# Optimization experiments

Measured on AMD Instinct MI355X. Metric: run time of the kernel, lower is better.

The kernel has to match this reference:

```python
import jax, jax.numpy as jnp
import numpy as np

B, C_IN, N = 32, 64, 128
OUT_FEATS = (64, 64, 128)
ATT_DIM = 64
EPS = 1e-5  # torch BatchNorm default


def _bn(x, g, b, m, v):
    # eval-mode BatchNorm over channel axis 1 (running stats m, v)
    shape = (1, -1) + (1,) * (x.ndim - 2)
    inv = g / jnp.sqrt(v + EPS)
    return (x - m.reshape(shape)) * inv.reshape(shape) + b.reshape(shape)


def setup_inputs() -> dict:
    key = jax.random.key(0)
    ks = iter(jax.random.split(key, 48))

    def w(shape, scale=0.05):
        return jax.random.normal(next(ks), shape, jnp.float32) * scale

    inp = {"features": jax.random.normal(next(ks), (B, C_IN, N), jnp.float32)}
    in_dims = (2 * C_IN, OUT_FEATS[0], OUT_FEATS[1])
    for li in range(3):
        o, ci = OUT_FEATS[li], in_dims[li]
        inp[f"w{li}"] = w((o, ci))                  # Conv2d 1x1, no bias (BN)
        inp[f"g{li}"] = 1.0 + w((o,))               # BN gamma
        inp[f"b{li}"] = w((o,))                     # BN beta
        inp[f"m{li}"] = w((o,))                     # BN running mean
        inp[f"v{li}"] = 1.0 + 0.1 * jax.random.uniform(next(ks), (o,), jnp.float32)
    inp["wa0"] = w((ATT_DIM, OUT_FEATS[-1]))        # attention conv (no bias)
    inp["ga"] = 1.0 + w((ATT_DIM,))
    inp["ba"] = w((ATT_DIM,))
    inp["ma"] = w((ATT_DIM,))
    inp["va"] = 1.0 + 0.1 * jax.random.uniform(next(ks), (ATT_DIM,), jnp.float32)
    inp["wa1"] = w((1, ATT_DIM))                    # final attention conv (bias)
    inp["ba1"] = w((1,))
    inp["wsc"] = w((OUT_FEATS[-1], C_IN))           # shortcut Conv1d (no bias)
    inp["gsc"] = 1.0 + w((OUT_FEATS[-1],))
    inp["bsc"] = w((OUT_FEATS[-1],))
    inp["msc"] = w((OUT_FEATS[-1],))
    inp["vsc"] = 1.0 + 0.1 * jax.random.uniform(next(ks), (OUT_FEATS[-1],), jnp.float32)
    return inp


def reference(features, w0, g0, b0, m0, v0, w1, g1, b1, m1, v1,
              w2, g2, b2, m2, v2, wa0, ga, ba, ma, va, wa1, ba1,
              wsc, gsc, bsc, msc, vsc):
    n = features.shape[-1]
    # neighbor index table: row i lists all j != i, shape (N, N-1)
    base = jnp.broadcast_to(jnp.arange(n)[None, :], (n, n))
    idx = jnp.where(base >= jnp.arange(n)[:, None], base + 1, base)[:, :-1]
    x_i = features[:, :, :, None]                   # (B,C,N,1)
    x_j = features[:, :, idx]                       # (B,C,N,N-1) gather
    x = jnp.concatenate([jnp.broadcast_to(x_i, x_j.shape), x_j - x_i], axis=1)  # (B,2C,N,N-1)
    for w_, g_, b_, m_, v_ in ((w0, g0, b0, m0, v0), (w1, g1, b1, m1, v1), (w2, g2, b2, m2, v2)):
        x = jnp.einsum('oc,bcnk->bonk', w_, x)      # 1x1 conv
        x = jax.nn.relu(_bn(x, g_, b_, m_, v_))
    # attention pooling over neighbor axis k
    a = jax.nn.relu(_bn(jnp.einsum('oc,bcnk->bonk', wa0, x), ga, ba, ma, va))
    logits = jnp.einsum('oc,bcnk->bonk', wa1, a) + ba1.reshape(1, 1, 1, 1)
    attw = jax.nn.softmax(logits[:, 0], axis=-1)    # (B,N,N-1)
    fts = jnp.einsum('bcnk,bnk->bcn', x, attw)      # (B,C_out,N)
    # shortcut branch (in_feat != out_feats[-1])
    sc = _bn(jnp.einsum('oc,bcn->bon', wsc, features), gsc, bsc, msc, vsc)
    return jax.nn.relu(sc + fts)
```

## Files before the change

### kernel.cpp

```cpp
#include <hip/hip_runtime.h>

typedef unsigned short u16;
typedef short short8 __attribute__((ext_vector_type(8)));
typedef float floatx4 __attribute__((ext_vector_type(4)));
typedef __bf16 bf16x2 __attribute__((ext_vector_type(2)));

#define MFMA16(a, b, c) __builtin_amdgcn_mfma_f32_16x16x32_bf16((a), (b), (c), 0, 0, 0)

#define W1F_OFF   0u
#define B1F_OFF   8192u
#define W2F_OFF   8448u
#define B2F_OFF   24832u
#define WA0F_OFF  25344u
#define BAF_OFF   41728u
#define WA1F_OFF  41984u
#define BA1F_OFF  42240u
#define P_OFF     42496u
#define Q_OFF     1091072u
#define SC_OFF    2139648u
#define WS_TOTAL  4236800u

__device__ __align__(256) char g_ws[WS_TOTAL];

#define LD0 72
#define LD2 136

__device__ __forceinline__ float bits2f(unsigned u) {
  union { unsigned i; float f; } v; v.i = u; return v.f;
}
__device__ __forceinline__ unsigned f2bits(float f) {
  union { float f; unsigned i; } v; v.f = f; return v.i;
}
__device__ __forceinline__ u16 f2bf(float f) {
  return (u16)((f2bits(f) + 0x8000u) >> 16);
}
__device__ __forceinline__ unsigned pack2relu(float a, float b) {
#if __has_builtin(__builtin_amdgcn_cvt_pk_bf16_f32)
  union { bf16x2 h; unsigned u; } cv;
  cv.h = __builtin_amdgcn_cvt_pk_bf16_f32(fmaxf(a, 0.f), fmaxf(b, 0.f));
  return cv.u;
#else
  unsigned lo = (f2bits(fmaxf(a, 0.f)) + 0x8000u) >> 16;
  unsigned hi = (f2bits(fmaxf(b, 0.f)) + 0x8000u) & 0xffff0000u;
  return lo | hi;
#endif
}

__global__ __launch_bounds__(256) void k_pre(
    const float* __restrict__ feat, const float* __restrict__ w0,
    const float* __restrict__ g0, const float* __restrict__ b0, const float* __restrict__ m0, const float* __restrict__ v0,
    const float* __restrict__ w1, const float* __restrict__ g1, const float* __restrict__ b1, const float* __restrict__ m1, const float* __restrict__ v1,
    const float* __restrict__ w2, const float* __restrict__ g2, const float* __restrict__ b2, const float* __restrict__ m2, const float* __restrict__ v2,
    const float* __restrict__ wa0, const float* __restrict__ ga, const float* __restrict__ ba, const float* __restrict__ ma, const float* __restrict__ va,
    const float* __restrict__ wa1, const float* __restrict__ ba1,
    const float* __restrict__ wsc, const float* __restrict__ gsc, const float* __restrict__ bsc, const float* __restrict__ msc, const float* __restrict__ vsc)
{
  __shared__ float smem[9600];
  const int t = threadIdx.x;
  char* ws = g_ws;
  const int blk = blockIdx.x;

  if (blk == 512) {
    float* fs1 = smem; float* fs2 = smem + 64; float* fsa = smem + 192;
    if (t < 64) {
      float s;
      s = g1[t] * rsqrtf(v1[t] + 1e-5f); fs1[t] = s; ((float*)(ws + B1F_OFF))[t] = b1[t] - m1[t] * s;
      s = ga[t] * rsqrtf(va[t] + 1e-5f); fsa[t] = s; ((float*)(ws + BAF_OFF))[t] = ba[t] - ma[t] * s;
      ((float*)(ws + WA1F_OFF))[t] = wa1[t];
    }
    if (t < 128) { float s = g2[t] * rsqrtf(v2[t] + 1e-5f); fs2[t] = s; ((float*)(ws + B2F_OFF))[t] = b2[t] - m2[t] * s; }
    if (t == 0) ((float*)(ws + BA1F_OFF))[0] = ba1[0];
    __syncthreads();
    u16* W1f = (u16*)(ws + W1F_OFF);
    u16* W2f = (u16*)(ws + W2F_OFF);
    u16* Wa0f = (u16*)(ws + WA0F_OFF);
    for (int i = t; i < 4096; i += 256) W1f[i]  = f2bf(fs1[i >> 6] * w1[i]);
    for (int i = t; i < 8192; i += 256) W2f[i]  = f2bf(fs2[i >> 6] * w2[i]);
    for (int i = t; i < 8192; i += 256) Wa0f[i] = f2bf(fsa[i >> 7] * wa0[i]);
    return;
  }

  const int sub = blk & 255;
  const int b = sub >> 3, n0 = (sub & 7) << 4;
  float* Xs  = smem;
  float* Wsm = smem + 1280;

  {
    const int c = t >> 2, j = (t & 3) << 2;
    *(float4*)(Xs + c * 20 + j) = *(const float4*)(feat + b * 8192 + c * 128 + n0 + j);
  }

  if (blk < 256) {
    #pragma unroll
    for (int r = 0; r < 8; r++) {
      const int i = (r * 256 + t) * 4;
      float4 v = *(const float4*)(w0 + i);
      const int o = i >> 7, c = i & 127;
      float* d = Wsm + o * 129 + c;
      d[0] = v.x; d[1] = v.y; d[2] = v.z; d[3] = v.w;
    }
    __syncthreads();
    const int o = t & 63, nb = (t >> 6) << 2;
    const float s  = g0[o] * rsqrtf(v0[o] + 1e-5f);
    const float tt = b0[o] - m0[o] * s;
    const float* wr = Wsm + o * 129;
    float dA0=0.f,dA1=0.f,dA2=0.f,dA3=0.f,dB0=0.f,dB1=0.f,dB2=0.f,dB3=0.f;
    #pragma unroll
    for (int c = 0; c < 64; c++) {
      const float a = wr[c], e = wr[64 + c];
      const float4 x = *(const float4*)(Xs + c * 20 + nb);
      dA0 += a * x.x; dA1 += a * x.y; dA2 += a * x.z; dA3 += a * x.w;
      dB0 += e * x.x; dB1 += e * x.y; dB2 += e * x.z; dB3 += e * x.w;
    }
    float* Pp = (float*)(ws + P_OFF) + (b * 128 + n0 + nb) * 64 + o;
    float* Qp = (float*)(ws + Q_OFF) + (b * 128 + n0 + nb) * 64 + o;
    Pp[0]   = s * dB0; Pp[64]  = s * dB1; Pp[128] = s * dB2; Pp[192] = s * dB3;
    Qp[0]   = s * (dA0 - dB0) + tt; Qp[64]  = s * (dA1 - dB1) + tt;
    Qp[128] = s * (dA2 - dB2) + tt; Qp[192] = s * (dA3 - dB3) + tt;
  } else {
    #pragma unroll
    for (int r = 0; r < 8; r++) {
      const int i = (r * 256 + t) * 4;
      float4 v = *(const float4*)(wsc + i);
      const int o = i >> 6, c = i & 63;
      float* d = Wsm + o * 65 + c;
      d[0] = v.x; d[1] = v.y; d[2] = v.z; d[3] = v.w;
    }
    __syncthreads();
    const int o = t & 127, h = (t >> 7) << 3;
    const float s  = gsc[o] * rsqrtf(vsc[o] + 1e-5f);
    const float tt = bsc[o] - msc[o] * s;
    const float* wr = Wsm + o * 65;
    float d0=0.f,d1=0.f,d2=0.f,d3=0.f,d4=0.f,d5=0.f,d6=0.f,d7=0.f;
    #pragma unroll
    for (int c = 0; c < 64; c++) {
      const float a = wr[c];
      const float4 x0 = *(const float4*)(Xs + c * 20 + h);
      const float4 x1 = *(const float4*)(Xs + c * 20 + h + 4);
      d0 += a * x0.x; d1 += a * x0.y; d2 += a * x0.z; d3 += a * x0.w;
      d4 += a * x1.x; d5 += a * x1.y; d6 += a * x1.z; d7 += a * x1.w;
    }
    float* SCp = (float*)(ws + SC_OFF) + (b * 128 + n0 + h) * 128 + o;
    SCp[0]   = s * d0 + tt; SCp[128] = s * d1 + tt; SCp[256] = s * d2 + tt; SCp[384] = s * d3 + tt;
    SCp[512] = s * d4 + tt; SCp[640] = s * d5 + tt; SCp[768] = s * d6 + tt; SCp[896] = s * d7 + tt;
  }
}

__global__ __launch_bounds__(256, 4) void k_main(float* __restrict__ out)
{
  __shared__ alignas(16) u16 buf[18432];
  __shared__ float parts[4][128];
  __shared__ float attws[128];

  const int blk = blockIdx.x, b = blk >> 7, n = blk & 127, t = threadIdx.x;
  const char* ws = g_ws;
  const float* Pb  = (const float*)(ws + P_OFF);
  const float* Qb  = (const float*)(ws + Q_OFF);
  const float* SCb = (const float*)(ws + SC_OFF);
  const u16*   W1f = (const u16*)(ws + W1F_OFF);
  const float* b1f = (const float*)(ws + B1F_OFF);
  const u16*   W2f = (const u16*)(ws + W2F_OFF);
  const float* b2f = (const float*)(ws + B2F_OFF);
  const u16*   Wa0f= (const u16*)(ws + WA0F_OFF);
  const float* baf = (const float*)(ws + BAF_OFF);
  const float* wa1f= (const float*)(ws + WA1F_OFF);
  const float  ba1v= *(const float*)(ws + BA1F_OFF);

  u16* H1 = buf + 9216;
  u16* H2 = buf;

  const int lane = t & 63, wid = t >> 6, quad = lane >> 4, l16 = lane & 15;
  const int koff = quad * 8;

  {
    const float* Qr = Qb + blk * 64;
    const float4 q0a = *(const float4*)(Qr + koff);
    const float4 q0b = *(const float4*)(Qr + koff + 4);
    const float4 q1a = *(const float4*)(Qr + 32 + koff);
    const float4 q1b = *(const float4*)(Qr + 32 + koff + 4);
    short8 bfr[2][2];
    #pragma unroll
    for (int et2 = 0; et2 < 2; et2++) {
      const int e = wid * 32 + et2 * 16 + l16;
      const int j = (e < 127) ? ((e < n) ? e : (e + 1)) : n;
      const float* Pr = Pb + (((b << 7) + j) << 6);
      const float4 p0a = *(const float4*)(Pr + koff);
      const float4 p0b = *(const float4*)(Pr + koff + 4);
      const float4 p1a = *(const float4*)(Pr + 32 + koff);
      const float4 p1b = *(const float4*)(Pr + 32 + koff + 4);
      union { short8 s; uint4 u; } c0, c1;
      c0.u.x = pack2relu(q0a.x + p0a.x, q0a.y + p0a.y);
      c0.u.y = pack2relu(q0a.z + p0a.z, q0a.w + p0a.w);
      c0.u.z = pack2relu(q0b.x + p0b.x, q0b.y + p0b.y);
      c0.u.w = pack2relu(q0b.z + p0b.z, q0b.w + p0b.w);
      c1.u.x = pack2relu(q1a.x + p1a.x, q1a.y + p1a.y);
      c1.u.y = pack2relu(q1a.z + p1a.z, q1a.w + p1a.w);
      c1.u.z = pack2relu(q1b.x + p1b.x, q1b.y + p1b.y);
      c1.u.w = pack2relu(q1b.z + p1b.z, q1b.w + p1b.w);
      bfr[et2][0] = c0.s; bfr[et2][1] = c1.s;
    }
    uint2 sv[4][2];
    #pragma unroll
    for (int mt = 0; mt < 4; mt++) {
      const float4 bb = *(const float4*)(b1f + mt * 16 + quad * 4);
      floatx4 binit; binit[0] = bb.x; binit[1] = bb.y; binit[2] = bb.z; binit[3] = bb.w;
      const short8 a0 = *(const short8*)(W1f + (mt * 16 + l16) * 64 + koff);
      const short8 a1 = *(const short8*)(W1f + (mt * 16 + l16) * 64 + 32 + koff);
      #pragma unroll
      for (int et2 = 0; et2 < 2; et2++) {
        floatx4 a = binit;
        a = MFMA16(a0, bfr[et2][0], a);
        a = MFMA16(a1, bfr[et2][1], a);
        sv[mt][et2].x = pack2relu(a[0], a[1]);
        sv[mt][et2].y = pack2relu(a[2], a[3]);
      }
    }
    #pragma unroll
    for (int mt = 0; mt < 4; mt++)
      #pragma unroll
      for (int et2 = 0; et2 < 2; et2++)
        *(uint2*)(H1 + (wid * 32 + et2 * 16 + l16) * LD0 + mt * 16 + quad * 4) = sv[mt][et2];
  }
  __syncthreads();

  {
    const int wc = wid >> 1, we = wid & 1;
    short8 bfr[4][2];
    #pragma unroll
    for (int et2 = 0; et2 < 4; et2++) {
      const u16* br = H1 + (we * 64 + et2 * 16 + l16) * LD0 + koff;
      bfr[et2][0] = *(const short8*)(br);
      bfr[et2][1] = *(const short8*)(br + 32);
    }
    uint2 sv[4][4];
    #pragma unroll
    for (int mt = 0; mt < 4; mt++) {
      const int chb = wc * 64 + mt * 16;
      const float4 bb = *(const float4*)(b2f + chb + quad * 4);
      floatx4 binit; binit[0] = bb.x; binit[1] = bb.y; binit[2] = bb.z; binit[3] = bb.w;
      const short8 a0 = *(const short8*)(W2f + (chb + l16) * 64 + koff);
      const short8 a1 = *(const short8*)(W2f + (chb + l16) * 64 + 32 + koff);
      #pragma unroll
      for (int et2 = 0; et2 < 4; et2++) {
        floatx4 a = binit;
        a = MFMA16(a0, bfr[et2][0], a);
        a = MFMA16(a1, bfr[et2][1], a);
        sv[mt][et2].x = pack2relu(a[0], a[1]);
        sv[mt][et2].y = pack2relu(a[2], a[3]);
      }
    }
    __syncthreads();
    #pragma unroll
    for (int mt = 0; mt < 4; mt++)
      #pragma unroll
      for (int et2 = 0; et2 < 4; et2++)
        *(uint2*)(H2 + (we * 64 + et2 * 16 + l16) * LD2 + wc * 64 + mt * 16 + quad * 4) = sv[mt][et2];
  }
  __syncthreads();

  float scv = 0.f;
  if (t < 128) scv = SCb[blk * 128 + t];
  float* outp = out + ((b << 7) + (t & 127)) * 128 + n;

  {
    short8 bfr[2][4];
    #pragma unroll
    for (int et2 = 0; et2 < 2; et2++) {
      const u16* br = H2 + (wid * 32 + et2 * 16 + l16) * LD2 + koff;
      #pragma unroll
      for (int ks = 0; ks < 4; ks++)
        bfr[et2][ks] = *(const short8*)(br + ks * 32);
    }
    float p0 = 0.f, p1 = 0.f;
    #pragma unroll
    for (int mt = 0; mt < 4; mt++) {
      const float4 bb = *(const float4*)(baf + mt * 16 + quad * 4);
      const float4 wv = *(const float4*)(wa1f + mt * 16 + quad * 4);
      floatx4 binit; binit[0] = bb.x; binit[1] = bb.y; binit[2] = bb.z; binit[3] = bb.w;
      floatx4 ac0 = binit, ac1 = binit;
      #pragma unroll
      for (int ks = 0; ks < 4; ks++) {
        const short8 aa = *(const short8*)(Wa0f + (mt * 16 + l16) * 128 + ks * 32 + koff);
        ac0 = MFMA16(aa, bfr[0][ks], ac0);
        ac1 = MFMA16(aa, bfr[1][ks], ac1);
      }
      p0 += wv.x * fmaxf(ac0[0], 0.f) + wv.y * fmaxf(ac0[1], 0.f)
          + wv.z * fmaxf(ac0[2], 0.f) + wv.w * fmaxf(ac0[3], 0.f);
      p1 += wv.x * fmaxf(ac1[0], 0.f) + wv.y * fmaxf(ac1[1], 0.f)
          + wv.z * fmaxf(ac1[2], 0.f) + wv.w * fmaxf(ac1[3], 0.f);
    }
    p0 += __shfl_xor(p0, 16); p0 += __shfl_xor(p0, 32);
    p1 += __shfl_xor(p1, 16); p1 += __shfl_xor(p1, 32);
    if (quad == 0) {
      parts[0][wid * 32 + l16]      = p0;
      parts[0][wid * 32 + 16 + l16] = p1;
    }
  }
  __syncthreads();

  if (wid == 0) {
    float a0 = parts[0][lane] + ba1v;
    float a1 = (lane == 63) ? -1e30f : (parts[0][lane + 64] + ba1v);
    float mx = fmaxf(a0, a1);
    #pragma unroll
    for (int off = 32; off >= 1; off >>= 1) mx = fmaxf(mx, __shfl_xor(mx, off));
    float e0 = expf(a0 - mx), e1 = expf(a1 - mx);
    float sm = e0 + e1;
    #pragma unroll
    for (int off = 32; off >= 1; off >>= 1) sm += __shfl_xor(sm, off);
    float inv = 1.f / sm;
    attws[lane] = e0 * inv;
    attws[lane + 64] = e1 * inv;
  }
  __syncthreads();

  {
    const int chg = t & 15, eg = t >> 4;
    float fa[8];
    #pragma unroll
    for (int k = 0; k < 8; k++) fa[k] = 0.f;
    #pragma unroll
    for (int i = 0; i < 8; i++) {
      const int e = eg * 8 + i;
      const float w = attws[e];
      uint4 v = *(const uint4*)(H2 + e * LD2 + chg * 8);
      unsigned u;
      u = v.x; fa[0] += w * bits2f(u << 16); fa[1] += w * bits2f(u & 0xffff0000u);
      u = v.y; fa[2] += w * bits2f(u << 16); fa[3] += w * bits2f(u & 0xffff0000u);
      u = v.z; fa[4] += w * bits2f(u << 16); fa[5] += w * bits2f(u & 0xffff0000u);
      u = v.w; fa[6] += w * bits2f(u << 16); fa[7] += w * bits2f(u & 0xffff0000u);
    }
    #pragma unroll
    for (int k = 0; k < 8; k++) { fa[k] += __shfl_xor(fa[k], 16); fa[k] += __shfl_xor(fa[k], 32); }
    if (lane < 16) {
      #pragma unroll
      for (int k = 0; k < 8; k++) parts[wid][chg * 8 + k] = fa[k];
    }
  }
  __syncthreads();

  if (t < 128) {
    float fts = parts[0][t] + parts[1][t] + parts[2][t] + parts[3][t];
    *outp = fmaxf(scv + fts, 0.f);
  }
}

extern "C" void kernel_launch(void* const* d_in, const int* in_sizes, int n_in,
                              void* d_out, int out_size, void* d_ws, size_t ws_size,
                              hipStream_t stream)
{
  (void)d_ws; (void)ws_size; (void)in_sizes; (void)n_in; (void)out_size;
  const float* feat = (const float*)d_in[0];
  const float *w0 = (const float*)d_in[1],  *g0 = (const float*)d_in[2],  *b0 = (const float*)d_in[3],  *m0 = (const float*)d_in[4],  *v0 = (const float*)d_in[5];
  const float *w1 = (const float*)d_in[6],  *g1 = (const float*)d_in[7],  *b1 = (const float*)d_in[8],  *m1 = (const float*)d_in[9],  *v1 = (const float*)d_in[10];
  const float *w2 = (const float*)d_in[11], *g2 = (const float*)d_in[12], *b2 = (const float*)d_in[13], *m2 = (const float*)d_in[14], *v2 = (const float*)d_in[15];
  const float *wa0= (const float*)d_in[16], *ga = (const float*)d_in[17], *ba = (const float*)d_in[18], *ma = (const float*)d_in[19], *va = (const float*)d_in[20];
  const float *wa1= (const float*)d_in[21], *ba1= (const float*)d_in[22];
  const float *wsc= (const float*)d_in[23], *gsc= (const float*)d_in[24], *bsc= (const float*)d_in[25], *msc= (const float*)d_in[26], *vsc= (const float*)d_in[27];

  k_pre<<<dim3(513), dim3(256), 0, stream>>>(
      feat, w0, g0, b0, m0, v0, w1, g1, b1, m1, v1, w2, g2, b2, m2, v2,
      wa0, ga, ba, ma, va, wa1, ba1, wsc, gsc, bsc, msc, vsc);
  k_main<<<dim3(4096), dim3(256), 0, stream>>>((float*)d_out);
}
```

Before: 199.1 us.

## Make each wave own its neighbor rows end-to-end and tile P layout

Each wave now keeps its 32 neighbor rows in a private LDS region through layers 1, 2 and attention. The two block-wide barriers between those layers go away, and the layer-2 GEMM is split by rows instead of by channel halves. The P workspace is re-laid out into 8-channel tiles so each lane's gathered P loads are contiguous 32-byte chunks. The per-wave partial feature sums are combined through LDS atomics instead of a parts array. In exchange, each wave loads the full W2 itself.

```diff
diff --git a/kernel.cpp b/kernel.cpp
--- a/kernel.cpp
+++ b/kernel.cpp
@@ -21,9 +21,6 @@
 #define WS_TOTAL  4236800u
 
 __device__ __align__(256) char g_ws[WS_TOTAL];
-
-#define LD0 72
-#define LD2 136
 
 __device__ __forceinline__ float bits2f(unsigned u) {
   union { unsigned i; float f; } v; v.i = u; return v.f;
@@ -112,9 +109,9 @@
       dA0 += a * x.x; dA1 += a * x.y; dA2 += a * x.z; dA3 += a * x.w;
       dB0 += e * x.x; dB1 += e * x.y; dB2 += e * x.z; dB3 += e * x.w;
     }
-    float* Pp = (float*)(ws + P_OFF) + (b * 128 + n0 + nb) * 64 + o;
+    float* Pp = (float*)(ws + P_OFF) + (((b * 8 + (o >> 3)) << 7) + n0 + nb) * 8 + (o & 7);
     float* Qp = (float*)(ws + Q_OFF) + (b * 128 + n0 + nb) * 64 + o;
-    Pp[0]   = s * dB0; Pp[64]  = s * dB1; Pp[128] = s * dB2; Pp[192] = s * dB3;
+    Pp[0]  = s * dB0; Pp[8]  = s * dB1; Pp[16] = s * dB2; Pp[24] = s * dB3;
     Qp[0]   = s * (dA0 - dB0) + tt; Qp[64]  = s * (dA1 - dB1) + tt;
     Qp[128] = s * (dA2 - dB2) + tt; Qp[192] = s * (dA3 - dB3) + tt;
   } else {
@@ -148,9 +145,9 @@
 
 __global__ __launch_bounds__(256, 4) void k_main(float* __restrict__ out)
 {
-  __shared__ alignas(16) u16 buf[18432];
-  __shared__ float parts[4][128];
-  __shared__ float attws[128];
+  __shared__ alignas(16) u16 buf[17408];
+  __shared__ float logits[128];
+  __shared__ float ftsAcc[128];
 
   const int blk = blockIdx.x, b = blk >> 7, n = blk & 127, t = threadIdx.x;
   const char* ws = g_ws;
@@ -166,11 +163,15 @@
   const float* wa1f= (const float*)(ws + WA1F_OFF);
   const float  ba1v= *(const float*)(ws + BA1F_OFF);
 
-  u16* H1 = buf + 9216;
-  u16* H2 = buf;
-
   const int lane = t & 63, wid = t >> 6, quad = lane >> 4, l16 = lane & 15;
   const int koff = quad * 8;
+
+  u16* Hw = buf + wid * 4352;
+
+  if (t < 128) ftsAcc[t] = 0.f;
+  float scv = 0.f;
+  if (t < 128) scv = SCb[blk * 128 + t];
+  float* outp = out + ((b << 7) + (t & 127)) * 128 + n;
 
   {
     const float* Qr = Qb + blk * 64;
@@ -178,16 +179,17 @@
     const float4 q0b = *(const float4*)(Qr + koff + 4);
     const float4 q1a = *(const float4*)(Qr + 32 + koff);
     const float4 q1b = *(const float4*)(Qr + 32 + koff + 4);
+    const float* PT0 = Pb + ((b * 8 + quad) << 10);
+    const float* PT1 = Pb + ((b * 8 + quad + 4) << 10);
     short8 bfr[2][2];
     #pragma unroll
     for (int et2 = 0; et2 < 2; et2++) {
       const int e = wid * 32 + et2 * 16 + l16;
       const int j = (e < 127) ? ((e < n) ? e : (e + 1)) : n;
-      const float* Pr = Pb + (((b << 7) + j) << 6);
-      const float4 p0a = *(const float4*)(Pr + koff);
-      const float4 p0b = *(const float4*)(Pr + koff + 4);
-      const float4 p1a = *(const float4*)(Pr + 32 + koff);
-      const float4 p1b = *(const float4*)(Pr + 32 + koff + 4);
+      const float4 p0a = *(const float4*)(PT0 + j * 8);
+      const float4 p0b = *(const float4*)(PT0 + j * 8 + 4);
+      const float4 p1a = *(const float4*)(PT1 + j * 8);
+      const float4 p1b = *(const float4*)(PT1 + j * 8 + 4);
       union { short8 s; uint4 u; } c0, c1;
       c0.u.x = pack2relu(q0a.x + p0a.x, q0a.y + p0a.y);
       c0.u.y = pack2relu(q0a.z + p0a.z, q0a.w + p0a.w);
@@ -199,7 +201,6 @@
       c1.u.w = pack2relu(q1b.z + p1b.z, q1b.w + p1b.w);
       bfr[et2][0] = c0.s; bfr[et2][1] = c1.s;
     }
-    uint2 sv[4][2];
     #pragma unroll
     for (int mt = 0; mt < 4; mt++) {
       const float4 bb = *(const float4*)(b1f + mt * 16 + quad * 4);
@@ -211,62 +212,46 @@
         floatx4 a = binit;
         a = MFMA16(a0, bfr[et2][0], a);
         a = MFMA16(a1, bfr[et2][1], a);
-        sv[mt][et2].x = pack2relu(a[0], a[1]);
-        sv[mt][et2].y = pack2relu(a[2], a[3]);
+        uint2 sv;
+        sv.x = pack2relu(a[0], a[1]);
+        sv.y = pack2relu(a[2], a[3]);
+        *(uint2*)(Hw + (et2 * 16 + l16) * 72 + mt * 16 + quad * 4) = sv;
       }
     }
-    #pragma unroll
-    for (int mt = 0; mt < 4; mt++)
-      #pragma unroll
-      for (int et2 = 0; et2 < 2; et2++)
-        *(uint2*)(H1 + (wid * 32 + et2 * 16 + l16) * LD0 + mt * 16 + quad * 4) = sv[mt][et2];
-  }
-  __syncthreads();
-
-  {
-    const int wc = wid >> 1, we = wid & 1;
-    short8 bfr[4][2];
-    #pragma unroll
-    for (int et2 = 0; et2 < 4; et2++) {
-      const u16* br = H1 + (we * 64 + et2 * 16 + l16) * LD0 + koff;
+  }
+
+  {
+    short8 bfr[2][2];
+    #pragma unroll
+    for (int et2 = 0; et2 < 2; et2++) {
+      const u16* br = Hw + (et2 * 16 + l16) * 72 + koff;
       bfr[et2][0] = *(const short8*)(br);
       bfr[et2][1] = *(const short8*)(br + 32);
     }
-    uint2 sv[4][4];
-    #pragma unroll
-    for (int mt = 0; mt < 4; mt++) {
-      const int chb = wc * 64 + mt * 16;
-      const float4 bb = *(const float4*)(b2f + chb + quad * 4);
+    #pragma unroll
+    for (int mt = 0; mt < 8; mt++) {
+      const float4 bb = *(const float4*)(b2f + mt * 16 + quad * 4);
       floatx4 binit; binit[0] = bb.x; binit[1] = bb.y; binit[2] = bb.z; binit[3] = bb.w;
-      const short8 a0 = *(const short8*)(W2f + (chb + l16) * 64 + koff);
-      const short8 a1 = *(const short8*)(W2f + (chb + l16) * 64 + 32 + koff);
-      #pragma unroll
-      for (int et2 = 0; et2 < 4; et2++) {
+      const short8 a0 = *(const short8*)(W2f + (mt * 16 + l16) * 64 + koff);
+      const short8 a1 = *(const short8*)(W2f + (mt * 16 + l16) * 64 + 32 + koff);
+      #pragma unroll
+      for (int et2 = 0; et2 < 2; et2++) {
         floatx4 a = binit;
         a = MFMA16(a0, bfr[et2][0], a);
         a = MFMA16(a1, bfr[et2][1], a);
-        sv[mt][et2].x = pack2relu(a[0], a[1]);
-        sv[mt][et2].y = pack2relu(a[2], a[3]);
+        uint2 sv;
+        sv.x = pack2relu(a[0], a[1]);
+        sv.y = pack2relu(a[2], a[3]);
+        *(uint2*)(Hw + (et2 * 16 + l16) * 136 + mt * 16 + quad * 4) = sv;
       }
     }
-    __syncthreads();
-    #pragma unroll
-    for (int mt = 0; mt < 4; mt++)
-      #pragma unroll
-      for (int et2 = 0; et2 < 4; et2++)
-        *(uint2*)(H2 + (we * 64 + et2 * 16 + l16) * LD2 + wc * 64 + mt * 16 + quad * 4) = sv[mt][et2];
-  }
-  __syncthreads();
-
-  float scv = 0.f;
-  if (t < 128) scv = SCb[blk * 128 + t];
-  float* outp = out + ((b << 7) + (t & 127)) * 128 + n;
+  }
 
   {
     short8 bfr[2][4];
     #pragma unroll
     for (int et2 = 0; et2 < 2; et2++) {
-      const u16* br = H2 + (wid * 32 + et2 * 16 + l16) * LD2 + koff;
+      const u16* br = Hw + (et2 * 16 + l16) * 136 + koff;
       #pragma unroll
       for (int ks = 0; ks < 4; ks++)
         bfr[et2][ks] = *(const short8*)(br + ks * 32);
@@ -292,15 +277,15 @@
     p0 += __shfl_xor(p0, 16); p0 += __shfl_xor(p0, 32);
     p1 += __shfl_xor(p1, 16); p1 += __shfl_xor(p1, 32);
     if (quad == 0) {
-      parts[0][wid * 32 + l16]      = p0;
-      parts[0][wid * 32 + 16 + l16] = p1;
+      logits[wid * 32 + l16]      = p0;
+      logits[wid * 32 + 16 + l16] = p1;
     }
   }
   __syncthreads();
 
   if (wid == 0) {
-    float a0 = parts[0][lane] + ba1v;
-    float a1 = (lane == 63) ? -1e30f : (parts[0][lane + 64] + ba1v);
+    float a0 = logits[lane] + ba1v;
+    float a1 = (lane == 63) ? -1e30f : (logits[lane + 64] + ba1v);
     float mx = fmaxf(a0, a1);
     #pragma unroll
     for (int off = 32; off >= 1; off >>= 1) mx = fmaxf(mx, __shfl_xor(mx, off));
@@ -309,21 +294,21 @@
     #pragma unroll
     for (int off = 32; off >= 1; off >>= 1) sm += __shfl_xor(sm, off);
     float inv = 1.f / sm;
-    attws[lane] = e0 * inv;
-    attws[lane + 64] = e1 * inv;
+    logits[lane] = e0 * inv;
+    logits[lane + 64] = e1 * inv;
   }
   __syncthreads();
 
   {
-    const int chg = t & 15, eg = t >> 4;
+    const int chg = l16;
     float fa[8];
     #pragma unroll
     for (int k = 0; k < 8; k++) fa[k] = 0.f;
     #pragma unroll
     for (int i = 0; i < 8; i++) {
-      const int e = eg * 8 + i;
-      const float w = attws[e];
-      uint4 v = *(const uint4*)(H2 + e * LD2 + chg * 8);
+      const int el = quad * 8 + i;
+      const float w = logits[wid * 32 + el];
+      uint4 v = *(const uint4*)(Hw + el * 136 + chg * 8);
       unsigned u;
       u = v.x; fa[0] += w * bits2f(u << 16); fa[1] += w * bits2f(u & 0xffff0000u);
       u = v.y; fa[2] += w * bits2f(u << 16); fa[3] += w * bits2f(u & 0xffff0000u);
@@ -334,15 +319,12 @@
     for (int k = 0; k < 8; k++) { fa[k] += __shfl_xor(fa[k], 16); fa[k] += __shfl_xor(fa[k], 32); }
     if (lane < 16) {
       #pragma unroll
-      for (int k = 0; k < 8; k++) parts[wid][chg * 8 + k] = fa[k];
+      for (int k = 0; k < 8; k++) atomicAdd(&ftsAcc[chg * 8 + k], fa[k]);
     }
   }
   __syncthreads();
 
-  if (t < 128) {
-    float fts = parts[0][t] + parts[1][t] + parts[2][t] + parts[3][t];
-    *outp = fmaxf(scv + fts, 0.f);
-  }
+  if (t < 128) *outp = fmaxf(scv + ftsAcc[t], 0.f);
 }
 
 extern "C" void kernel_launch(void* const* d_in, const int* in_sizes, int n_in,
```

Result: no change. 202.0 us (+1.4%).
